# Kernel optimization log

Hardware: AMD Instinct MI355X
Metric: run time of the kernel (lower is better)

Reference implementation:

```python
import jax, jax.numpy as jnp
import numpy as np

CEN_WEIGHT = 0.5
EPS = 1e-10


def setup_inputs() -> dict:
    key = jax.random.key(0)
    k1, k2, k3 = jax.random.split(key, 3)
    num_mods, N, B = 2, 500000, 100
    logits = jax.random.normal(k1, (num_mods, N, B), dtype=jnp.float32)
    preds = jax.nn.softmax(logits, axis=-1)  # module expects probability bins
    labs = jax.random.randint(k2, (num_mods, N), 0, B).astype(jnp.int64)
    cen_in = jax.random.randint(k3, (num_mods, N), 0, 2).astype(jnp.int32)
    return {"preds": preds, "labs": labs, "cen_in": cen_in}


def _mod_loss(p, lab, cen, labs0):
    # p: [N, B] probabilities; lab: [N] bin labels for this mod;
    # cen: [N] censor flags; labs0: [N] times from mod 0 (as in original code)
    N, B = p.shape
    uncen_mask = (cen == 0)
    cen_mask = (cen == 1)
    num_uncen = jnp.sum(uncen_mask).astype(p.dtype)
    num_cen = jnp.sum(cen_mask).astype(p.dtype)

    # uncensored: -mean log p[i, lab_i]
    g = jnp.take_along_axis(p, lab[:, None].astype(jnp.int32), axis=1)[:, 0]
    uncen_loss = -jnp.sum(jnp.where(uncen_mask, jnp.log(g + EPS), 0.0)) \
        / jnp.maximum(1.0, num_uncen)

    # censored: -log(sum_{j > t_i} p[i, j]); suffix-sum replaces the python
    # loop over unique times (grouped sums of per-example terms are identical)
    suffix = jnp.flip(jnp.cumsum(jnp.flip(p, axis=1), axis=1), axis=1)  # sum_{j>=k}
    suffix = jnp.concatenate([suffix, jnp.zeros((N, 1), p.dtype)], axis=1)
    t1 = (labs0 + 1)[:, None].astype(jnp.int32)
    s = jnp.take_along_axis(suffix, t1, axis=1)[:, 0]
    cen_loss = jnp.sum(jnp.where(cen_mask, -jnp.log(s + EPS), 0.0)) \
        / jnp.maximum(1.0, num_cen)

    n = jnp.asarray(N, p.dtype)
    return (num_uncen / n) * uncen_loss + (num_cen / n) * cen_loss * CEN_WEIGHT


def reference(preds, labs, cen_in):
    labs0 = labs[0]
    losses = jax.vmap(_mod_loss, in_axes=(0, 0, 0, None))(preds, labs, cen_in, labs0)
    return jnp.sum(losses)
```

## Files before the change

kernel.cpp:

```cpp
#include <hip/hip_runtime.h>
#include <hip/hip_bf16.h>


#define HSL_EPS 1e-10f
#define NBLK 2048

__global__ __launch_bounds__(256, 4) void hsl_main(
    const float* __restrict__ preds,
    const int*   __restrict__ labs,
    const int*   __restrict__ cen,
    double*       __restrict__ bsums,
    unsigned int* __restrict__ bcnts,
    long long N, int use_atomic)
{
    const long long R = 2LL * N;
    const int q = threadIdx.x & 3;
    const long long g0 = ((long long)blockIdx.x * blockDim.x + threadIdx.x) >> 2;
    const long long ng = ((long long)gridDim.x * blockDim.x) >> 2;

    double usum[2] = {0.0, 0.0};
    double csum[2] = {0.0, 0.0};
    unsigned int ucnt[2] = {0u, 0u};
    unsigned int ccnt[2] = {0u, 0u};

    for (long long r = g0; r < R; r += ng) {
        const int m = (r >= N) ? 1 : 0;
        const long long i0 = r - (long long)m * N;
        const int lab = labs[r];
        const int t1  = labs[i0] + 1;
        const int c   = cen[r];
        const float* rowp = preds + r * 100;

        float4 v[7];
        #pragma unroll
        for (int k = 0; k < 6; ++k)
            v[k] = *(const float4*)(rowp + 4 * q + 16 * k);
        v[6] = *(const float4*)(rowp + 96);

        float sp = 0.0f, gp = 0.0f;
        const int jb = 4 * q;
        #pragma unroll
        for (int k = 0; k < 6; ++k) {
            #pragma unroll
            for (int e = 0; e < 4; ++e) {
                const int j = jb + 16 * k + e;
                const float p = ((const float*)&v[k])[e];
                sp += (j >= t1) ? p : 0.0f;
                gp  = (j == lab) ? p : gp;
            }
        }
        if (q == 0) {
            #pragma unroll
            for (int e = 0; e < 4; ++e) {
                const int j = 96 + e;
                const float p = ((const float*)&v[6])[e];
                sp += (j >= t1) ? p : 0.0f;
                gp  = (j == lab) ? p : gp;
            }
        }

        sp += __shfl_xor(sp, 1, 64); sp += __shfl_xor(sp, 2, 64);
        gp += __shfl_xor(gp, 1, 64); gp += __shfl_xor(gp, 2, 64);

        if (q == 0) {
            if (c == 0) { usum[m] += (double)logf(gp + HSL_EPS); ucnt[m]++; }
            else        { csum[m] += (double)logf(sp + HSL_EPS); ccnt[m]++; }
        }
    }

    #pragma unroll
    for (int off = 32; off > 0; off >>= 1) {
        usum[0] += __shfl_down(usum[0], off, 64);
        csum[0] += __shfl_down(csum[0], off, 64);
        usum[1] += __shfl_down(usum[1], off, 64);
        csum[1] += __shfl_down(csum[1], off, 64);
        ucnt[0] += __shfl_down(ucnt[0], off, 64);
        ccnt[0] += __shfl_down(ccnt[0], off, 64);
        ucnt[1] += __shfl_down(ucnt[1], off, 64);
        ccnt[1] += __shfl_down(ccnt[1], off, 64);
    }

    __shared__ double sh_sums[4][4];
    __shared__ unsigned int sh_cnts[4][4];
    const int waveInBlk = threadIdx.x >> 6;
    const int lane = threadIdx.x & 63;
    if (lane == 0) {
        sh_sums[waveInBlk][0] = usum[0]; sh_sums[waveInBlk][1] = csum[0];
        sh_sums[waveInBlk][2] = usum[1]; sh_sums[waveInBlk][3] = csum[1];
        sh_cnts[waveInBlk][0] = ucnt[0]; sh_cnts[waveInBlk][1] = ccnt[0];
        sh_cnts[waveInBlk][2] = ucnt[1]; sh_cnts[waveInBlk][3] = ccnt[1];
    }
    __syncthreads();
    if (threadIdx.x < 4) {
        const int slot = threadIdx.x;
        double s = 0.0; unsigned int k = 0u;
        for (int w = 0; w < 4; ++w) { s += sh_sums[w][slot]; k += sh_cnts[w][slot]; }
        if (use_atomic) {
            atomicAdd(&bsums[slot], s);
            if (k) atomicAdd(&bcnts[slot], k);
        } else {
            bsums[slot * NBLK + blockIdx.x] = s;
            bcnts[slot * NBLK + blockIdx.x] = k;
        }
    }
}

__global__ __launch_bounds__(256) void hsl_final(
    const double* __restrict__ bsums,
    const unsigned int* __restrict__ bcnts,
    float* __restrict__ out, long long N, int nblk)
{
    double s[4] = {0.0, 0.0, 0.0, 0.0};
    double kc[4] = {0.0, 0.0, 0.0, 0.0};
    if (nblk > 0) {
        for (int b = threadIdx.x; b < nblk; b += 256) {
            #pragma unroll
            for (int slot = 0; slot < 4; ++slot) {
                s[slot]  += bsums[slot * nblk + b];
                kc[slot] += (double)bcnts[slot * nblk + b];
            }
        }
    } else if (threadIdx.x == 0) {
        #pragma unroll
        for (int slot = 0; slot < 4; ++slot) {
            s[slot] = bsums[slot]; kc[slot] = (double)bcnts[slot];
        }
    }

    #pragma unroll
    for (int off = 32; off > 0; off >>= 1) {
        #pragma unroll
        for (int slot = 0; slot < 4; ++slot) {
            s[slot]  += __shfl_down(s[slot],  off, 64);
            kc[slot] += __shfl_down(kc[slot], off, 64);
        }
    }

    __shared__ double sh[4][8];
    const int waveInBlk = threadIdx.x >> 6;
    const int lane = threadIdx.x & 63;
    if (lane == 0) {
        #pragma unroll
        for (int slot = 0; slot < 4; ++slot) {
            sh[waveInBlk][slot]     = s[slot];
            sh[waveInBlk][4 + slot] = kc[slot];
        }
    }
    __syncthreads();
    if (threadIdx.x == 0) {
        double fs[4], fk[4];
        #pragma unroll
        for (int slot = 0; slot < 4; ++slot) {
            fs[slot] = sh[0][slot] + sh[1][slot] + sh[2][slot] + sh[3][slot];
            fk[slot] = sh[0][4+slot] + sh[1][4+slot] + sh[2][4+slot] + sh[3][4+slot];
        }
        float total = 0.0f;
        const float n = (float)N;
        for (int m = 0; m < 2; ++m) {
            const float nu = (float)fk[2 * m + 0];
            const float nc = (float)fk[2 * m + 1];
            const float us = (float)fs[2 * m + 0];
            const float cs = (float)fs[2 * m + 1];
            const float uncen_loss = -us / fmaxf(1.0f, nu);
            const float cen_loss   = -cs / fmaxf(1.0f, nc);
            total += (nu / n) * uncen_loss + (nc / n) * cen_loss * 0.5f;
        }
        out[0] = total;
    }
}

extern "C" void kernel_launch(void* const* d_in, const int* in_sizes, int n_in,
                              void* d_out, int out_size, void* d_ws, size_t ws_size,
                              hipStream_t stream)
{
    const float* preds = (const float*)d_in[0];
    const int*   labs  = (const int*)d_in[1];
    const int*   cen   = (const int*)d_in[2];
    float* out = (float*)d_out;

    const long long N = (long long)(in_sizes[1] / 2);

    const size_t need = (size_t)4 * NBLK * sizeof(double)
                      + (size_t)4 * NBLK * sizeof(unsigned int);

    if (ws_size >= need) {
        double*       bsums = (double*)d_ws;
        unsigned int* bcnts = (unsigned int*)((char*)d_ws + (size_t)4 * NBLK * sizeof(double));
        hsl_main<<<NBLK, 256, 0, stream>>>(preds, labs, cen, bsums, bcnts, N, 0);
        hsl_final<<<1, 256, 0, stream>>>(bsums, bcnts, out, N, NBLK);
    } else {
        double*       sums = (double*)d_ws;
        unsigned int* cnts = (unsigned int*)((char*)d_ws + 32);
        hipMemsetAsync(d_ws, 0, 48, stream);
        hsl_main<<<NBLK, 256, 0, stream>>>(preds, labs, cen, sums, cnts, N, 1);
        hsl_final<<<1, 256, 0, stream>>>(sums, cnts, out, N, 0);
    }
}
```

Measured before the change: 528.6 us.

## Skip unneeded row loads: single gather for uncensored, half-row sums for censored

Measured after the change: 480.6 us. -9.1%, faster.

```diff
diff --git a/kernel.cpp b/kernel.cpp
--- a/kernel.cpp
+++ b/kernel.cpp
@@ -5,13 +5,13 @@
 #define HSL_EPS 1e-10f
 #define NBLK 2048
 
-__global__ __launch_bounds__(256, 4) void hsl_main(
+__global__ __launch_bounds__(256, 8) void hsl_main(
     const float* __restrict__ preds,
     const int*   __restrict__ labs,
     const int*   __restrict__ cen,
     double*       __restrict__ bsums,
     unsigned int* __restrict__ bcnts,
-    long long N, int use_atomic)
+    long long N)
 {
     const long long R = 2LL * N;
     const int q = threadIdx.x & 3;
@@ -26,45 +26,42 @@
     for (long long r = g0; r < R; r += ng) {
         const int m = (r >= N) ? 1 : 0;
         const long long i0 = r - (long long)m * N;
+        const int c   = cen[r];
         const int lab = labs[r];
         const int t1  = labs[i0] + 1;
-        const int c   = cen[r];
         const float* rowp = preds + r * 100;
 
-        float4 v[7];
-        #pragma unroll
-        for (int k = 0; k < 6; ++k)
-            v[k] = *(const float4*)(rowp + 4 * q + 16 * k);
-        v[6] = *(const float4*)(rowp + 96);
+        if (c == 0) {
+            const float gp = rowp[lab];
+            if (q == 0) { usum[m] += (double)logf(gp + HSL_EPS); ucnt[m]++; }
+        } else {
+            const bool pre = (t1 <= 50);
+            const int b4 = pre ? 0 : (t1 >> 2);
+            const float4* rowp4 = (const float4*)rowp;
 
-        float sp = 0.0f, gp = 0.0f;
-        const int jb = 4 * q;
-        #pragma unroll
-        for (int k = 0; k < 6; ++k) {
+            float sp = 0.0f;
             #pragma unroll
-            for (int e = 0; e < 4; ++e) {
-                const int j = jb + 16 * k + e;
-                const float p = ((const float*)&v[k])[e];
-                sp += (j >= t1) ? p : 0.0f;
-                gp  = (j == lab) ? p : gp;
+            for (int k = 0; k < 4; ++k) {
+                const int f4 = b4 + 4 * k + q;
+                const bool issue = pre ? (4 * f4 < t1) : (f4 <= 24);
+                if (issue) {
+                    const float4 v = rowp4[f4];
+                    #pragma unroll
+                    for (int e = 0; e < 4; ++e) {
+                        const int j = 4 * f4 + e;
+                        const float p = ((const float*)&v)[e];
+                        const bool use = pre ? (j < t1) : (j >= t1);
+                        sp += use ? p : 0.0f;
+                    }
+                }
             }
-        }
-        if (q == 0) {
-            #pragma unroll
-            for (int e = 0; e < 4; ++e) {
-                const int j = 96 + e;
-                const float p = ((const float*)&v[6])[e];
-                sp += (j >= t1) ? p : 0.0f;
-                gp  = (j == lab) ? p : gp;
+            sp += __shfl_xor(sp, 1, 64);
+            sp += __shfl_xor(sp, 2, 64);
+            if (q == 0) {
+                const float s = pre ? (1.0f - sp) : sp;
+                csum[m] += (double)logf(s + HSL_EPS);
+                ccnt[m]++;
             }
-        }
-
-        sp += __shfl_xor(sp, 1, 64); sp += __shfl_xor(sp, 2, 64);
-        gp += __shfl_xor(gp, 1, 64); gp += __shfl_xor(gp, 2, 64);
-
-        if (q == 0) {
-            if (c == 0) { usum[m] += (double)logf(gp + HSL_EPS); ucnt[m]++; }
-            else        { csum[m] += (double)logf(sp + HSL_EPS); ccnt[m]++; }
         }
     }
 
@@ -95,13 +92,8 @@
         const int slot = threadIdx.x;
         double s = 0.0; unsigned int k = 0u;
         for (int w = 0; w < 4; ++w) { s += sh_sums[w][slot]; k += sh_cnts[w][slot]; }
-        if (use_atomic) {
-            atomicAdd(&bsums[slot], s);
-            if (k) atomicAdd(&bcnts[slot], k);
-        } else {
-            bsums[slot * NBLK + blockIdx.x] = s;
-            bcnts[slot * NBLK + blockIdx.x] = k;
-        }
+        bsums[slot * NBLK + blockIdx.x] = s;
+        bcnts[slot * NBLK + blockIdx.x] = k;
     }
 }
 
@@ -112,18 +104,11 @@
 {
     double s[4] = {0.0, 0.0, 0.0, 0.0};
     double kc[4] = {0.0, 0.0, 0.0, 0.0};
-    if (nblk > 0) {
-        for (int b = threadIdx.x; b < nblk; b += 256) {
-            #pragma unroll
-            for (int slot = 0; slot < 4; ++slot) {
-                s[slot]  += bsums[slot * nblk + b];
-                kc[slot] += (double)bcnts[slot * nblk + b];
-            }
-        }
-    } else if (threadIdx.x == 0) {
+    for (int b = threadIdx.x; b < nblk; b += 256) {
         #pragma unroll
         for (int slot = 0; slot < 4; ++slot) {
-            s[slot] = bsums[slot]; kc[slot] = (double)bcnts[slot];
+            s[slot]  += bsums[slot * nblk + b];
+            kc[slot] += (double)bcnts[slot * nblk + b];
         }
     }
 
@@ -180,19 +165,9 @@
 
     const long long N = (long long)(in_sizes[1] / 2);
 
-    const size_t need = (size_t)4 * NBLK * sizeof(double)
-                      + (size_t)4 * NBLK * sizeof(unsigned int);
+    double*       bsums = (double*)d_ws;
+    unsigned int* bcnts = (unsigned int*)((char*)d_ws + (size_t)4 * NBLK * sizeof(double));
 
-    if (ws_size >= need) {
-        double*       bsums = (double*)d_ws;
-        unsigned int* bcnts = (unsigned int*)((char*)d_ws + (size_t)4 * NBLK * sizeof(double));
-        hsl_main<<<NBLK, 256, 0, stream>>>(preds, labs, cen, bsums, bcnts, N, 0);
-        hsl_final<<<1, 256, 0, stream>>>(bsums, bcnts, out, N, NBLK);
-    } else {
-        double*       sums = (double*)d_ws;
-        unsigned int* cnts = (unsigned int*)((char*)d_ws + 32);
-        hipMemsetAsync(d_ws, 0, 48, stream);
-        hsl_main<<<NBLK, 256, 0, stream>>>(preds, labs, cen, sums, cnts, N, 1);
-        hsl_final<<<1, 256, 0, stream>>>(sums, cnts, out, N, 0);
-    }
+    hsl_main<<<NBLK, 256, 0, stream>>>(preds, labs, cen, bsums, bcnts, N);
+    hsl_final<<<1, 256, 0, stream>>>(bsums, bcnts, out, N, NBLK);
 }
```
